# Performance work log

Hardware: AMD Instinct MI355X
Metric: run time of the kernel (lower is better)

The kernel has to match this reference:

```python
import jax, jax.numpy as jnp
import numpy as np

B, S, T = 512, 1024, 50


def setup_inputs() -> dict:
    key = jax.random.key(0)
    k1, k2, k3, k4, k5, k6, k7 = jax.random.split(key, 7)
    token_scores = jax.random.normal(k1, (B, S, T), dtype=jnp.float32)
    tags = jax.random.randint(k2, (B, S), 0, T, dtype=jnp.int64)
    # left-contiguous mask: each sequence has a random valid length >= 1
    lengths = jax.random.randint(k3, (B,), 1, S + 1)
    token_mask = (jnp.arange(S)[None, :] < lengths[:, None]).astype(jnp.int32)
    transitions = jax.random.normal(k4, (T, T), dtype=jnp.float32) * 0.1
    start_transitions = jax.random.normal(k5, (T,), dtype=jnp.float32) * 0.1
    end_transitions = jax.random.normal(k6, (T,), dtype=jnp.float32) * 0.1
    return {
        "token_scores": token_scores,
        "tags": tags,
        "token_mask": token_mask,
        "transitions": transitions,
        "start_transitions": start_transitions,
        "end_transitions": end_transitions,
    }


def _crf_log_likelihood(token_scores, tags, token_mask, transitions,
                        start_transitions, end_transitions):
    # token_scores: [B,S,T], tags: [B,S] int, token_mask: [B,S] {0,1}
    maskf = token_mask.astype(token_scores.dtype)
    maskb = token_mask.astype(bool)

    # ---- numerator: score of the gold tag path ----
    emit = jnp.take_along_axis(token_scores, tags[..., None], axis=2)[..., 0]  # [B,S]
    emit_sum = jnp.sum(emit * maskf, axis=1)
    trans_sum = jnp.sum(transitions[tags[:, :-1], tags[:, 1:]] * maskf[:, 1:], axis=1)
    start_score = start_transitions[tags[:, 0]]
    last_idx = jnp.sum(token_mask, axis=1).astype(jnp.int32) - 1          # [B]
    last_tags = jnp.take_along_axis(tags, last_idx[:, None], axis=1)[:, 0]
    end_score = end_transitions[last_tags]
    numerator = start_score + emit_sum + trans_sum + end_score            # [B]

    # ---- denominator: log partition via forward algorithm (scan over time) ----
    alpha0 = start_transitions[None, :] + token_scores[:, 0]              # [B,T]
    logits_rest = jnp.swapaxes(token_scores[:, 1:], 0, 1)                 # [S-1,B,T]
    mask_rest = jnp.swapaxes(maskb[:, 1:], 0, 1)                          # [S-1,B]

    def step(alpha, xs):
        logit_t, m_t = xs                                                 # [B,T], [B]
        # inner[b, i, j] = alpha[b,i] + transitions[i,j] + logit_t[b,j]
        inner = alpha[:, :, None] + transitions[None, :, :] + logit_t[:, None, :]
        new_alpha = jax.nn.logsumexp(inner, axis=1)                       # [B,T]
        alpha = jnp.where(m_t[:, None], new_alpha, alpha)
        return alpha, None

    alpha, _ = jax.lax.scan(step, alpha0, (logits_rest, mask_rest))
    denominator = jax.nn.logsumexp(alpha + end_transitions[None, :], axis=1)  # [B]

    return jnp.sum(numerator - denominator)  # scalar, summed over batch


def reference(token_scores, tags, token_mask, transitions,
              start_transitions, end_transitions):
    batch_size = token_scores.shape[0]
    ll = _crf_log_likelihood(token_scores, tags, token_mask, transitions,
                             start_transitions, end_transitions)
    return -ll / float(batch_size)
```

## Files before the change

kernel.cpp:

```cpp
#include <hip/hip_runtime.h>
#include <math.h>

#define CB 512
#define CS 1024
#define CT 50
#define PF 4

typedef float v2f __attribute__((ext_vector_type(2)));

__global__ void zero_out_kernel(float* out) { out[0] = 0.0f; }

__device__ __forceinline__ void wave_fence() {
    __builtin_amdgcn_wave_barrier();
    asm volatile("" ::: "memory");
}

__device__ __forceinline__ int lane0_bits(float v) {
    return __builtin_amdgcn_readlane(__float_as_int(v), 0);
}

template <int CTRL>
__device__ __forceinline__ float qperm(float v) {
    return __int_as_float(__builtin_amdgcn_update_dpp(
        0, __float_as_int(v), CTRL, 0xf, 0xf, false));
}

__global__ __launch_bounds__(128, 1) void crf_scan_kernel(
    const float* __restrict__ scores,
    const int*   __restrict__ tags,
    const int*   __restrict__ mask,
    const float* __restrict__ trans,
    const float* __restrict__ start_tr,
    const float* __restrict__ end_tr,
    float* __restrict__ out)
{
    const int b    = blockIdx.x;
    const int tid  = threadIdx.x;
    const int w    = tid >> 6;
    const int lane = tid & 63;
    const int xl   = (lane < CT) ? lane : 0;
    const int g    = lane & 3;
    const int m    = lane >> 2;
    const bool selb0 = (lane & 1) != 0;
    const bool selb1 = (lane & 2) != 0;

    __shared__ __attribute__((aligned(16))) float sTrans[CT * CT];
    __shared__ __attribute__((aligned(16))) float sP2[2][64];
    __shared__ __attribute__((aligned(16))) float sA[64];
    __shared__ __attribute__((aligned(16))) float sB[64];
    __shared__ float sLZ[2], sN[2];

    for (int k = tid; k < CT * CT; k += 128) sTrans[k] = trans[k];
    __syncthreads();

    v2f EC0[16], EC1[16];
    {
        const int i0 = 16 * g, s0 = 4 * m;
        #pragma unroll
        for (int k = 0; k < 16; ++k) {
            const int i = i0 + k;
            float e[4] = {0.f, 0.f, 0.f, 0.f};
            if (i < CT) {
                #pragma unroll
                for (int c = 0; c < 4; ++c) {
                    const int s = s0 + c;
                    if (s < CT)
                        e[c] = __expf(w == 0 ? sTrans[i * CT + s]
                                             : sTrans[s * CT + i]);
                }
            }
            EC0[k] = (v2f){e[0], e[1]};
            EC1[k] = (v2f){e[2], e[3]};
        }
    }

    const int* mrow = mask + (size_t)b * CS;
    int len = 0;
    for (int t = lane; t < CS; t += 64) len += mrow[t];
    #pragma unroll
    for (int off = 32; off; off >>= 1) len += __shfl_xor(len, off);

    const float* srow = scores + (size_t)b * CS * CT;
    const float* sx   = srow + xl;

    const int tm    = (len - 1) >> 1;
    const int count = (w == 0) ? tm : ((len >= 2) ? (len - 2 - tm) : 0);
    const int base  = (w == 0) ? 1 : (len - 2);
    const int dir   = (w == 0) ? 1 : -1;

    float st;
    if (w == 0) {
        st = (lane < CT) ? __expf(start_tr[lane] + sx[0]) : 0.f;
    } else {
        st = (lane < CT)
            ? ((len >= 2) ? __expf(end_tr[lane] + sx[(size_t)(len - 1) * CT])
                          : __expf(end_tr[lane]))
            : 0.f;
    }
    int kexp = 0;
    float* sP = sP2[w];
    const float* sPq = sP + 16 * g;

    #define STEP(EX)                                                        \
    {                                                                       \
        sP[lane] = st;                                                      \
        wave_fence();                                                       \
        const float4 p0 = *(const float4*)&sPq[0];                          \
        const float4 p1 = *(const float4*)&sPq[4];                          \
        const float4 p2 = *(const float4*)&sPq[8];                          \
        const float4 p3 = *(const float4*)&sPq[12];                         \
        wave_fence();    \
        float pv[16] = {p0.x,p0.y,p0.z,p0.w, p1.x,p1.y,p1.z,p1.w,           \
                        p2.x,p2.y,p2.z,p2.w, p3.x,p3.y,p3.z,p3.w};          \
        v2f a0 = {0.f,0.f}, a1 = {0.f,0.f};                                 \
        _Pragma("unroll")                                                   \
        for (int kk = 0; kk < 16; ++kk) {                                   \
            const v2f t2 = {pv[kk], pv[kk]};                                \
            a0 = __builtin_elementwise_fma(t2, EC0[kk], a0);                \
            a1 = __builtin_elementwise_fma(t2, EC1[kk], a1);                \
        }                                                                   \
        a0.x += qperm<0xB1>(a0.x); a0.y += qperm<0xB1>(a0.y);               \
        a1.x += qperm<0xB1>(a1.x); a1.y += qperm<0xB1>(a1.y);               \
        a0.x += qperm<0x4E>(a0.x); a0.y += qperm<0x4E>(a0.y);               \
        a1.x += qperm<0x4E>(a1.x); a1.y += qperm<0x4E>(a1.y);               \
        const float o01 = selb0 ? a0.y : a0.x;                              \
        const float o23 = selb0 ? a1.y : a1.x;                              \
        st = (selb1 ? o23 : o01) * (EX);                                    \
    }

    #define RENORM()                                                        \
    {                                                                       \
        int sb = lane0_bits(st);                                            \
        int e  = (sb >> 23) & 0xff;                                         \
        kexp  += e - 127;                                                   \
        st    *= __int_as_float((254 - e) << 23);                           \
    }

    float xpf[PF];
    #pragma unroll
    for (int k = 0; k < PF; ++k) {
        int idx = base + dir * k;
        if (idx < 0) idx = 0;
        xpf[k] = sx[(size_t)idx * CT];
    }
    int k = 0;
    while (k + PF <= count) {
        float exk[PF];
        #pragma unroll
        for (int j = 0; j < PF; ++j) exk[j] = __expf(xpf[j]);
        #pragma unroll
        for (int j = 0; j < PF; ++j) {
            int idx = base + dir * (k + PF + j);
            if (idx < 0) idx = 0;
            xpf[j] = sx[(size_t)idx * CT];
        }
        RENORM();
        STEP(exk[0]); STEP(exk[1]); STEP(exk[2]); STEP(exk[3]);
        k += PF;
    }
    for (int r = 0; k < count; ++k, ++r) {
        float e = __expf(xpf[r]);
        RENORM();
        STEP(e);
    }
    if (w == 1 && len >= 2) { RENORM(); STEP(1.0f); }
    RENORM();
    #undef STEP
    #undef RENORM

    if (w == 0) sA[lane] = (lane < CT) ? st : 0.0f;
    else        sB[lane] = (lane < CT) ? st : 0.0f;
    if (lane == 0) sLZ[w] = (float)kexp * 0.6931471805599453f;
    __syncthreads();

    const int* trow = tags + (size_t)b * CS;
    float nsum = 0.0f;
    for (int t = tid; t < CS; t += 128) {
        if (t < len) {
            int tg = trow[t];
            nsum += srow[(size_t)t * CT + tg];
            if (t >= 1) nsum += sTrans[trow[t - 1] * CT + tg];
        }
    }
    #pragma unroll
    for (int off = 32; off; off >>= 1) nsum += __shfl_xor(nsum, off);
    if (lane == 0) sN[w] = nsum;

    float den = 0.0f;
    if (w == 0) {
        float vp = sA[lane] * sB[lane];
        #pragma unroll
        for (int off = 32; off; off >>= 1) vp += __shfl_xor(vp, off);
        den = sLZ[0] + sLZ[1] + __logf(vp);
    }
    __syncthreads();

    if (tid == 0) {
        float num = sN[0] + sN[1] + start_tr[trow[0]] + end_tr[trow[len - 1]];
        atomicAdd(out, (den - num) * (1.0f / CB));
    }
}

extern "C" void kernel_launch(void* const* d_in, const int* in_sizes, int n_in,
                              void* d_out, int out_size, void* d_ws, size_t ws_size,
                              hipStream_t stream) {
    const float* scores   = (const float*)d_in[0];
    const int*   tags     = (const int*)d_in[1];
    const int*   mask     = (const int*)d_in[2];
    const float* trans    = (const float*)d_in[3];
    const float* start_tr = (const float*)d_in[4];
    const float* end_tr   = (const float*)d_in[5];
    float* out = (float*)d_out;

    zero_out_kernel<<<1, 1, 0, stream>>>(out);
    crf_scan_kernel<<<CB, 128, 0, stream>>>(scores, tags, mask, trans,
                                            start_tr, end_tr, out);
}
```

Before: 261.6 us.

## Keep CRF forward state quad-replicated and shorten the per-step dependency chain

The serial forward recurrence now keeps each quad's four tag values replicated as vector registers. Only one lane per quad writes a float4 to LDS, and the emission exponentials are broadcast within the quad via DPP quad permutes, which removes the per-step select chain. The 16-term FMA reduction is split into two independent accumulators to shorten the dependent latency. Renormalisation is folded into a scale factor applied once per block of steps, and the prefetch depth goes from 4 to 8. The trade-off is more register pressure and larger value growth between renormalisations, which could risk overflow if scores were large.

```diff
diff --git a/kernel.cpp b/kernel.cpp
--- a/kernel.cpp
+++ b/kernel.cpp
@@ -4,7 +4,7 @@
 #define CB 512
 #define CS 1024
 #define CT 50
-#define PF 4
+#define PF 8
 
 typedef float v2f __attribute__((ext_vector_type(2)));
 
@@ -38,11 +38,8 @@
     const int tid  = threadIdx.x;
     const int w    = tid >> 6;
     const int lane = tid & 63;
-    const int xl   = (lane < CT) ? lane : 0;
     const int g    = lane & 3;
     const int m    = lane >> 2;
-    const bool selb0 = (lane & 1) != 0;
-    const bool selb1 = (lane & 2) != 0;
 
     __shared__ __attribute__((aligned(16))) float sTrans[CT * CT];
     __shared__ __attribute__((aligned(16))) float sP2[2][64];
@@ -57,8 +54,8 @@
     {
         const int i0 = 16 * g, s0 = 4 * m;
         #pragma unroll
-        for (int k = 0; k < 16; ++k) {
-            const int i = i0 + k;
+        for (int kk = 0; kk < 16; ++kk) {
+            const int i = i0 + kk;
             float e[4] = {0.f, 0.f, 0.f, 0.f};
             if (i < CT) {
                 #pragma unroll
@@ -69,8 +66,8 @@
                                              : sTrans[s * CT + i]);
                 }
             }
-            EC0[k] = (v2f){e[0], e[1]};
-            EC1[k] = (v2f){e[2], e[3]};
+            EC0[kk] = (v2f){e[0], e[1]};
+            EC1[kk] = (v2f){e[2], e[3]};
         }
     }
 
@@ -81,6 +78,7 @@
     for (int off = 32; off; off >>= 1) len += __shfl_xor(len, off);
 
     const float* srow = scores + (size_t)b * CS * CT;
+    const int xl      = (lane < CT) ? lane : 0;
     const float* sx   = srow + xl;
 
     const int tm    = (len - 1) >> 1;
@@ -88,52 +86,69 @@
     const int base  = (w == 0) ? 1 : (len - 2);
     const int dir   = (w == 0) ? 1 : -1;
 
-    float st;
-    if (w == 0) {
-        st = (lane < CT) ? __expf(start_tr[lane] + sx[0]) : 0.f;
-    } else {
-        st = (lane < CT)
-            ? ((len >= 2) ? __expf(end_tr[lane] + sx[(size_t)(len - 1) * CT])
-                          : __expf(end_tr[lane]))
-            : 0.f;
-    }
+    v2f C01, C23;
+    {
+        float c4[4];
+        #pragma unroll
+        for (int c = 0; c < 4; ++c) {
+            const int s = 4 * m + c;
+            if (s < CT) {
+                if (w == 0)      c4[c] = __expf(start_tr[s] + srow[s]);
+                else if (len >= 2) c4[c] = __expf(end_tr[s] + srow[(size_t)(len - 1) * CT + s]);
+                else             c4[c] = __expf(end_tr[s]);
+            } else c4[c] = 0.f;
+        }
+        C01 = (v2f){c4[0], c4[1]};
+        C23 = (v2f){c4[2], c4[3]};
+    }
+
     int kexp = 0;
+    float scl = 1.0f;
     float* sP = sP2[w];
     const float* sPq = sP + 16 * g;
 
-    #define STEP(EX)                                                        \
+    #define STEP(EXJ)                                                       \
     {                                                                       \
-        sP[lane] = st;                                                      \
+        if ((lane & 3) == 0)                                                \
+            *(float4*)&sP[lane] = make_float4(C01.x, C01.y, C23.x, C23.y);  \
         wave_fence();                                                       \
         const float4 p0 = *(const float4*)&sPq[0];                          \
         const float4 p1 = *(const float4*)&sPq[4];                          \
         const float4 p2 = *(const float4*)&sPq[8];                          \
         const float4 p3 = *(const float4*)&sPq[12];                         \
-        wave_fence();    \
+        const float exj = (EXJ);                                            \
+        const float e0 = qperm<0x00>(exj), e1 = qperm<0x55>(exj);           \
+        const float e2 = qperm<0xAA>(exj), e3 = qperm<0xFF>(exj);           \
         float pv[16] = {p0.x,p0.y,p0.z,p0.w, p1.x,p1.y,p1.z,p1.w,           \
                         p2.x,p2.y,p2.z,p2.w, p3.x,p3.y,p3.z,p3.w};          \
-        v2f a0 = {0.f,0.f}, a1 = {0.f,0.f};                                 \
+        v2f a0a={0.f,0.f}, a0b={0.f,0.f}, a1a={0.f,0.f}, a1b={0.f,0.f};     \
         _Pragma("unroll")                                                   \
-        for (int kk = 0; kk < 16; ++kk) {                                   \
+        for (int kk = 0; kk < 8; ++kk) {                                    \
             const v2f t2 = {pv[kk], pv[kk]};                                \
-            a0 = __builtin_elementwise_fma(t2, EC0[kk], a0);                \
-            a1 = __builtin_elementwise_fma(t2, EC1[kk], a1);                \
+            a0a = __builtin_elementwise_fma(t2, EC0[kk], a0a);              \
+            a1a = __builtin_elementwise_fma(t2, EC1[kk], a1a);              \
         }                                                                   \
-        a0.x += qperm<0xB1>(a0.x); a0.y += qperm<0xB1>(a0.y);               \
-        a1.x += qperm<0xB1>(a1.x); a1.y += qperm<0xB1>(a1.y);               \
-        a0.x += qperm<0x4E>(a0.x); a0.y += qperm<0x4E>(a0.y);               \
-        a1.x += qperm<0x4E>(a1.x); a1.y += qperm<0x4E>(a1.y);               \
-        const float o01 = selb0 ? a0.y : a0.x;                              \
-        const float o23 = selb0 ? a1.y : a1.x;                              \
-        st = (selb1 ? o23 : o01) * (EX);                                    \
-    }
-
-    #define RENORM()                                                        \
+        _Pragma("unroll")                                                   \
+        for (int kk = 8; kk < 16; ++kk) {                                   \
+            const v2f t2 = {pv[kk], pv[kk]};                                \
+            a0b = __builtin_elementwise_fma(t2, EC0[kk], a0b);              \
+            a1b = __builtin_elementwise_fma(t2, EC1[kk], a1b);              \
+        }                                                                   \
+        v2f A0 = a0a + a0b, A1 = a1a + a1b;                                 \
+        A0.x += qperm<0xB1>(A0.x); A0.y += qperm<0xB1>(A0.y);               \
+        A1.x += qperm<0xB1>(A1.x); A1.y += qperm<0xB1>(A1.y);               \
+        A0.x += qperm<0x4E>(A0.x); A0.y += qperm<0x4E>(A0.y);               \
+        A1.x += qperm<0x4E>(A1.x); A1.y += qperm<0x4E>(A1.y);               \
+        C01 = A0 * (v2f){e0, e1};                                           \
+        C23 = A1 * (v2f){e2, e3};                                           \
+    }
+
+    #define TAKE_SCALE()                                                    \
     {                                                                       \
-        int sb = lane0_bits(st);                                            \
+        int sb = lane0_bits(C01.x);                                         \
         int e  = (sb >> 23) & 0xff;                                         \
         kexp  += e - 127;                                                   \
-        st    *= __int_as_float((254 - e) << 23);                           \
+        scl    = __int_as_float((254 - e) << 23);                           \
     }
 
     float xpf[PF];
@@ -154,19 +169,41 @@
             if (idx < 0) idx = 0;
             xpf[j] = sx[(size_t)idx * CT];
         }
-        RENORM();
+        TAKE_SCALE();
+        exk[0] *= scl;
         STEP(exk[0]); STEP(exk[1]); STEP(exk[2]); STEP(exk[3]);
+        STEP(exk[4]); STEP(exk[5]); STEP(exk[6]); STEP(exk[7]);
         k += PF;
     }
-    for (int r = 0; k < count; ++k, ++r) {
-        float e = __expf(xpf[r]);
-        RENORM();
-        STEP(e);
-    }
-    if (w == 1 && len >= 2) { RENORM(); STEP(1.0f); }
-    RENORM();
+    if (k < count) {
+        TAKE_SCALE();
+        int r = 0;
+        for (; k < count; ++k, ++r) {
+            float ex = __expf(xpf[r]);
+            if (r == 0) ex *= scl;
+            STEP(ex);
+        }
+    }
+    if (w == 1 && len >= 2) {
+        TAKE_SCALE();
+        STEP(scl);
+    }
+    {
+        int sb = lane0_bits(C01.x);
+        int e  = (sb >> 23) & 0xff;
+        kexp  += e - 127;
+        float s2 = __int_as_float((254 - e) << 23);
+        C01 *= s2; C23 *= s2;
+    }
     #undef STEP
-    #undef RENORM
+    #undef TAKE_SCALE
+
+    float st;
+    {
+        const float o01 = (lane & 1) ? C01.y : C01.x;
+        const float o23 = (lane & 1) ? C23.y : C23.x;
+        st = (lane & 2) ? o23 : o01;
+    }
 
     if (w == 0) sA[lane] = (lane < CT) ? st : 0.0f;
     else        sB[lane] = (lane < CT) ? st : 0.0f;
```

New measurement: 294.8 us. 1.13x slower.
